# Kernel optimization log

Hardware: AMD Instinct MI355X
Metric: run time of the kernel (lower is better)

The kernel has to match this reference:

```python
import jax, jax.numpy as jnp
import numpy as np

CROP_H, CROP_W = 14, 14
EXTRAP = 0.0


def setup_inputs() -> dict:
    key = jax.random.key(0)
    k1, k2, k3 = jax.random.split(key, 3)
    image = jax.random.normal(k1, (8, 256, 200, 200), dtype=jnp.float32)
    boxes = jax.random.uniform(k2, (512, 4), dtype=jnp.float32)  # normalized [y1,x1,y2,x2]
    box_indices = jax.random.randint(k3, (512,), 0, 8).astype(jnp.int32)
    return {"image": image, "boxes": boxes, "box_indices": box_indices}


def _crop_and_resize(image, boxes, box_indices, crop_h, crop_w, extrap):
    # TF-style crop_and_resize with bilinear sampling (matches crop_and_resize_cpu).
    B, C, H, W = image.shape
    N = boxes.shape[0]
    y1, x1, y2, x2 = boxes[:, 0], boxes[:, 1], boxes[:, 2], boxes[:, 3]
    h_scale = (y2 - y1) * (H - 1) / (crop_h - 1)
    w_scale = (x2 - x1) * (W - 1) / (crop_w - 1)
    in_y = y1[:, None] * (H - 1) + jnp.arange(crop_h, dtype=jnp.float32)[None, :] * h_scale[:, None]  # [N,ch]
    in_x = x1[:, None] * (W - 1) + jnp.arange(crop_w, dtype=jnp.float32)[None, :] * w_scale[:, None]  # [N,cw]
    valid_y = (in_y >= 0) & (in_y <= H - 1)  # [N,ch]
    valid_x = (in_x >= 0) & (in_x <= W - 1)  # [N,cw]

    y_floor = jnp.floor(in_y)
    x_floor = jnp.floor(in_x)
    ly = (in_y - y_floor)[:, :, None, None]  # [N,ch,1,1]
    lx = (in_x - x_floor)[:, None, :, None]  # [N,1,cw,1]
    y0 = jnp.clip(y_floor, 0, H - 1).astype(jnp.int32)
    y1i = jnp.clip(jnp.ceil(in_y), 0, H - 1).astype(jnp.int32)
    x0 = jnp.clip(x_floor, 0, W - 1).astype(jnp.int32)
    x1i = jnp.clip(jnp.ceil(in_x), 0, W - 1).astype(jnp.int32)

    b = box_indices.astype(jnp.int32)[:, None, None]  # [N,1,1]

    def gather(yi, xi):
        # advanced indices [N,ch,cw] separated by ':' slice -> result [N,ch,cw,C]
        return image[b, :, yi[:, :, None], xi[:, None, :]]

    tl = gather(y0, x0)
    tr = gather(y0, x1i)
    bl = gather(y1i, x0)
    br = gather(y1i, x1i)

    top = tl + (tr - tl) * lx
    bot = bl + (br - bl) * lx
    val = top + (bot - top) * ly  # [N,ch,cw,C]

    mask = (valid_y[:, :, None] & valid_x[:, None, :])[:, :, :, None]
    val = jnp.where(mask, val, jnp.float32(extrap))
    return jnp.transpose(val, (0, 3, 1, 2))  # [N,C,ch,cw]


def reference(image, boxes, box_indices):
    return _crop_and_resize(image, boxes, box_indices, CROP_H, CROP_W, EXTRAP)
```

## Files before the change

kernel.cpp:

```cpp
#include <hip/hip_runtime.h>

#define CROP_H 14
#define CROP_W 14
#define NBOX   512
#define CH     256
#define IMH    200
#define IMW    200
#define PLANE   (IMH * IMW)
#define NPOS    (CROP_H * CROP_W)
#define PER_BOX (CH * NPOS)
#define CHUNK   512
#define NCHUNKS (PER_BOX / CHUNK)

__global__ __launch_bounds__(256, 8) void CropAndResize_60146722013533_kernel(
    const float* __restrict__ image,
    const float* __restrict__ boxes,
    const int*   __restrict__ box_idx,
    float*       __restrict__ out)
{
    const int n = blockIdx.x;
    const int t = threadIdx.x;

    __shared__ int   sy0[CROP_H], sy1[CROP_H], sx0[CROP_W], sx1[CROP_W];
    __shared__ float sly[CROP_H], slx[CROP_W];
    __shared__ int   svy[CROP_H], svx[CROP_W];
    __shared__ int   sb;

    if (t < CROP_H + CROP_W) {
        const float by1 = boxes[n * 4 + 0];
        const float bx1 = boxes[n * 4 + 1];
        const float by2 = boxes[n * 4 + 2];
        const float bx2 = boxes[n * 4 + 3];
        if (t < CROP_H) {
            const int gy = t;
            float h_scale = (by2 - by1) * (float)(IMH - 1) / (float)(CROP_H - 1);
            float in_y = by1 * (float)(IMH - 1) + (float)gy * h_scale;
            svy[gy] = (in_y >= 0.0f && in_y <= (float)(IMH - 1)) ? 1 : 0;
            float yf = floorf(in_y);
            sly[gy] = in_y - yf;
            sy0[gy] = (int)fminf(fmaxf(yf, 0.0f), (float)(IMH - 1));
            sy1[gy] = (int)fminf(fmaxf(ceilf(in_y), 0.0f), (float)(IMH - 1));
        } else {
            const int gx = t - CROP_H;
            float w_scale = (bx2 - bx1) * (float)(IMW - 1) / (float)(CROP_W - 1);
            float in_x = bx1 * (float)(IMW - 1) + (float)gx * w_scale;
            svx[gx] = (in_x >= 0.0f && in_x <= (float)(IMW - 1)) ? 1 : 0;
            float xf = floorf(in_x);
            slx[gx] = in_x - xf;
            sx0[gx] = (int)fminf(fmaxf(xf, 0.0f), (float)(IMW - 1));
            sx1[gx] = (int)fminf(fmaxf(ceilf(in_x), 0.0f), (float)(IMW - 1));
        }
    }
    if (t == 0) sb = box_idx[n];
    __syncthreads();

    const int base = blockIdx.y * CHUNK;
    const float* __restrict__ img = image + (size_t)sb * CH * PLANE;
    float* __restrict__ ob = out + (size_t)n * PER_BOX + base + t;

    const int elem0 = base + t;
    const int elem1 = elem0 + 256;

    const int c0  = elem0 / NPOS;
    const int r0  = elem0 - c0 * NPOS;
    const int gy0 = r0 / CROP_W;
    const int gx0 = r0 - gy0 * CROP_W;
    const int x0a = sx0[gx0];
    const int xb0 = (x0a < IMW - 2) ? x0a : (IMW - 2);
    const float* p0 = img + (size_t)c0 * PLANE;
    const float* rt0 = p0 + sy0[gy0] * IMW + xb0;
    const float* rb0 = p0 + sy1[gy0] * IMW + xb0;

    const int c1  = elem1 / NPOS;
    const int r1  = elem1 - c1 * NPOS;
    const int gy1 = r1 / CROP_W;
    const int gx1 = r1 - gy1 * CROP_W;
    const int x1a = sx0[gx1];
    const int xb1 = (x1a < IMW - 2) ? x1a : (IMW - 2);
    const float* p1 = img + (size_t)c1 * PLANE;
    const float* rt1 = p1 + sy0[gy1] * IMW + xb1;
    const float* rb1 = p1 + sy1[gy1] * IMW + xb1;

    float2 vt0, vb0, vt1, vb1;
    __builtin_memcpy(&vt0, rt0, 8);
    __builtin_memcpy(&vb0, rb0, 8);
    __builtin_memcpy(&vt1, rt1, 8);
    __builtin_memcpy(&vb1, rb1, 8);

    {
        const int   x1i = sx1[gx0];
        const float ly  = sly[gy0];
        const float lx  = slx[gx0];
        const float tl = (x0a == xb0) ? vt0.x : vt0.y;
        const float tr = (x1i == xb0) ? vt0.x : vt0.y;
        const float bl = (x0a == xb0) ? vb0.x : vb0.y;
        const float br = (x1i == xb0) ? vb0.x : vb0.y;
        const float top = tl + (tr - tl) * lx;
        const float bot = bl + (br - bl) * lx;
        float val = top + (bot - top) * ly;
        if (!(svy[gy0] & svx[gx0])) val = 0.0f;
        __builtin_nontemporal_store(val, ob);
    }
    {
        const int   x1i = sx1[gx1];
        const float ly  = sly[gy1];
        const float lx  = slx[gx1];
        const float tl = (x1a == xb1) ? vt1.x : vt1.y;
        const float tr = (x1i == xb1) ? vt1.x : vt1.y;
        const float bl = (x1a == xb1) ? vb1.x : vb1.y;
        const float br = (x1i == xb1) ? vb1.x : vb1.y;
        const float top = tl + (tr - tl) * lx;
        const float bot = bl + (br - bl) * lx;
        float val = top + (bot - top) * ly;
        if (!(svy[gy1] & svx[gx1])) val = 0.0f;
        __builtin_nontemporal_store(val, ob + 256);
    }
}

extern "C" void kernel_launch(void* const* d_in, const int* in_sizes, int n_in,
                              void* d_out, int out_size, void* d_ws, size_t ws_size,
                              hipStream_t stream) {
    const float* image   = (const float*)d_in[0];
    const float* boxes   = (const float*)d_in[1];
    const int*   box_idx = (const int*)d_in[2];
    float* out = (float*)d_out;

    dim3 grid(NBOX, NCHUNKS, 1);
    dim3 block(256, 1, 1);
    CropAndResize_60146722013533_kernel<<<grid, block, 0, stream>>>(image, boxes, box_idx, out);
}
```

Baseline: 488.3 us.

## Permute box-to-block order so each XCD processes boxes from one image

Adds a small preprocessing kernel that builds a permutation of boxes so block x maps to image x mod 8, with overflow boxes placed in leftover slots. The main kernel reads its box index through this permutation. The intent is that round-robin workgroup dispatch across the chiplets sends same-image boxes to the same L2, improving gather reuse. It costs an extra launch and an indirect load per block.

```diff
diff --git a/kernel.cpp b/kernel.cpp
--- a/kernel.cpp
+++ b/kernel.cpp
@@ -3,6 +3,7 @@
 #define CROP_H 14
 #define CROP_W 14
 #define NBOX   512
+#define NIMG   8
 #define CH     256
 #define IMH    200
 #define IMW    200
@@ -12,13 +13,42 @@
 #define CHUNK   512
 #define NCHUNKS (PER_BOX / CHUNK)
 
+__global__ __launch_bounds__(512) void CropAndResize_perm_kernel(
+    const int* __restrict__ box_idx, int* __restrict__ perm)
+{
+    __shared__ int cnt[NIMG];
+    __shared__ int nfree;
+    __shared__ int freeslots[NBOX];
+    const int t = threadIdx.x;
+    if (t < NIMG) cnt[t] = 0;
+    if (t == 0) nfree = 0;
+    __syncthreads();
+
+    const int img = box_idx[t];
+    const int r   = atomicAdd(&cnt[img], 1);
+    const int slot = (r < NBOX / NIMG) ? (img + NIMG * r) : -1;
+    __syncthreads();
+
+    int myfree = -1;
+    if ((t >> 3) >= cnt[t & 7]) {
+        const int k = atomicAdd(&nfree, 1);
+        freeslots[k] = t;
+    }
+    if (slot < 0) myfree = atomicAdd(&nfree, -1);
+    __syncthreads();
+
+    if (slot >= 0) perm[slot] = t;
+    else           perm[freeslots[myfree - 1]] = t;
+}
+
 __global__ __launch_bounds__(256, 8) void CropAndResize_60146722013533_kernel(
     const float* __restrict__ image,
     const float* __restrict__ boxes,
     const int*   __restrict__ box_idx,
+    const int*   __restrict__ perm,
     float*       __restrict__ out)
 {
-    const int n = blockIdx.x;
+    const int n = perm[blockIdx.x];
     const int t = threadIdx.x;
 
     __shared__ int   sy0[CROP_H], sy1[CROP_H], sx0[CROP_W], sx1[CROP_W];
@@ -123,9 +153,14 @@
     const float* image   = (const float*)d_in[0];
     const float* boxes   = (const float*)d_in[1];
     const int*   box_idx = (const int*)d_in[2];
-    float* out = (float*)d_out;
+    float* out  = (float*)d_out;
+    int*   perm = (int*)d_ws;
+
+    CropAndResize_perm_kernel<<<dim3(1, 1, 1), dim3(NBOX, 1, 1), 0, stream>>>(
+        box_idx, perm);
 
     dim3 grid(NBOX, NCHUNKS, 1);
     dim3 block(256, 1, 1);
-    CropAndResize_60146722013533_kernel<<<grid, block, 0, stream>>>(image, boxes, box_idx, out);
+    CropAndResize_60146722013533_kernel<<<grid, block, 0, stream>>>(
+        image, boxes, box_idx, perm, out);
 }
```

Result: no change. 484.5 us (-0.8%).
